# Optimization experiments

Hardware: AMD Instinct MI355X
Metric: run time of the kernel (lower is better)

Reference implementation:

```python
import jax, jax.numpy as jnp
import numpy as np

D_MODEL, H, D_FF = 512, 8, 2048
DK = D_MODEL // H
EPS = 1e-5  # torch LayerNorm default


def layer_norm(x, g, b):
    m = jnp.mean(x, axis=-1, keepdims=True)
    v = jnp.mean((x - m) ** 2, axis=-1, keepdims=True)
    return (x - m) * jax.lax.rsqrt(v + EPS) * g + b


def setup_inputs() -> dict:
    key = jax.random.key(0)
    ks = jax.random.split(key, 10)
    B, S = 8, 2048
    s = lambda fan_in: 1.0 / np.sqrt(fan_in)
    return {
        "x": jax.random.normal(ks[0], (B, S, D_MODEL), jnp.float32),
        # per-head projections stacked: [h, d_model, dk] (bias-free Project)
        "wq": jax.random.uniform(ks[1], (H, D_MODEL, DK), jnp.float32, -s(D_MODEL), s(D_MODEL)),
        "wk": jax.random.uniform(ks[2], (H, D_MODEL, DK), jnp.float32, -s(D_MODEL), s(D_MODEL)),
        "wv": jax.random.uniform(ks[3], (H, D_MODEL, DK), jnp.float32, -s(D_MODEL), s(D_MODEL)),
        "wo": jax.random.uniform(ks[4], (D_MODEL, D_MODEL), jnp.float32, -s(D_MODEL), s(D_MODEL)),
        "w1": jax.random.uniform(ks[5], (D_MODEL, D_FF), jnp.float32, -s(D_MODEL), s(D_MODEL)),
        "b1": jax.random.uniform(ks[6], (D_FF,), jnp.float32, -s(D_MODEL), s(D_MODEL)),
        "w2": jax.random.uniform(ks[7], (D_FF, D_MODEL), jnp.float32, -s(D_FF), s(D_FF)),
        "b2": jax.random.uniform(ks[8], (D_MODEL,), jnp.float32, -s(D_FF), s(D_FF)),
        "ln1_g": jnp.ones((D_MODEL,), jnp.float32),
        "ln1_b": jnp.zeros((D_MODEL,), jnp.float32),
        "ln2_g": jnp.ones((D_MODEL,), jnp.float32),
        "ln2_b": jnp.zeros((D_MODEL,), jnp.float32),
    }


def reference(x, wq, wk, wv, wo, w1, b1, w2, b2, ln1_g, ln1_b, ln2_g, ln2_b):
    B, S, D = x.shape
    # --- multi-head self-attention (8 per-head Linears fused into one einsum) ---
    q = jnp.einsum("bsd,hdk->bhsk", x, wq)
    k = jnp.einsum("bsd,hdk->bhsk", x, wk)
    v = jnp.einsum("bsd,hdk->bhsk", x, wv)
    score = jnp.einsum("bhsk,bhtk->bhst", q, k) * (1.0 / np.sqrt(DK))
    attn = jax.nn.softmax(score, axis=-1)
    heads = jnp.einsum("bhst,bhtk->bhsk", attn, v)
    concat = heads.transpose(0, 2, 1, 3).reshape(B, S, D)  # cat over heads
    mha = concat @ wo
    # dropout in eval mode -> identity
    x = layer_norm(mha + x, ln1_g, ln1_b)
    # --- feed-forward ---
    ffn = jax.nn.relu(x @ w1 + b1) @ w2 + b2
    return layer_norm(ffn + x, ln2_g, ln2_b)
```

## Files before the change

### kernel.cpp

```cpp
#include <hip/hip_runtime.h>
#include <hip/hip_bf16.h>
#include <math.h>


#define D_MODEL 512
#define NHEAD   8
#define DKH     64
#define SEQ     2048
#define BATCH   8
#define DFF     2048
#define MROWS   (BATCH * SEQ)
#define QKVLD   1536

typedef __bf16 bf16x8 __attribute__((ext_vector_type(8)));
typedef float  f32x4  __attribute__((ext_vector_type(4)));

__device__ __forceinline__ unsigned short f2bf(float f) {
    union { float f; unsigned u; } v; v.f = f;
    return (unsigned short)((v.u + 0x7FFFu + ((v.u >> 16) & 1u)) >> 16);
}

__device__ __forceinline__ unsigned cvtpk(float a, float b) {
    unsigned r;
    asm("v_cvt_pk_bf16_f32 %0, %1, %2" : "=v"(r) : "v"(a), "v"(b));
    return r;
}

__device__ __forceinline__ float fexp2(float x) {
    float r; asm("v_exp_f32 %0, %1" : "=v"(r) : "v"(x)); return r;
}

__device__ __forceinline__ f32x4 mfma16(bf16x8 a, bf16x8 b, f32x4 c) {
    return __builtin_amdgcn_mfma_f32_16x16x32_bf16(a, b, c, 0, 0, 0);
}

__device__ __forceinline__ void gld_lds16(const unsigned short* g, unsigned short* l) {
    __builtin_amdgcn_global_load_lds(
        (const __attribute__((address_space(1))) unsigned int*)g,
        (__attribute__((address_space(3))) unsigned int*)l, 16, 0, 0);
}

template<bool BIAS, bool RELU, bool RES, bool OUTF32>
__global__ __launch_bounds__(256)
void mfma_gemm(const unsigned short* __restrict__ Av,
               const unsigned short* __restrict__ Bt,
               const float* __restrict__ bias, const float* __restrict__ res,
               void* __restrict__ Cv, int Kdim, int lda, int ldc)
{
    __shared__ unsigned short As[2][128][32];
    __shared__ unsigned short Bs[2][128][32];

    const int tid  = threadIdx.x;
    const int lane = tid & 63;
    const int w    = tid >> 6;
    const int mq   = (w >> 1) << 6;
    const int nq   = (w & 1) << 6;
    const int lrow = lane & 15;
    const int g    = lane >> 4;
    const int lk   = g << 3;

    const int row0 = blockIdx.y << 7;
    const int col0 = blockIdx.x << 7;

    const int c0   = w << 5;
    const int srow = lane >> 2;
    const int scol = (lane & 3) << 3;
    const size_t aoff = (size_t)(row0 + c0 + srow) * lda  + scol;
    const size_t boff = (size_t)(col0 + c0 + srow) * Kdim + scol;

    auto stage = [&](int buf, int kt) {
        gld_lds16(Av + aoff + kt,                        &As[buf][c0     ][0]);
        gld_lds16(Av + aoff + (size_t)16 * lda  + kt,    &As[buf][c0 + 16][0]);
        gld_lds16(Bt + boff + kt,                        &Bs[buf][c0     ][0]);
        gld_lds16(Bt + boff + (size_t)16 * Kdim + kt,    &Bs[buf][c0 + 16][0]);
    };

    const f32x4 zero = {0.f, 0.f, 0.f, 0.f};
    f32x4 acc[4][4];
    #pragma unroll
    for (int i = 0; i < 4; ++i)
        #pragma unroll
        for (int j = 0; j < 4; ++j) acc[i][j] = zero;

    stage(0, 0);
    __syncthreads();

    int cur = 0;
    for (int kt = 0; kt < Kdim; kt += 32) {
        if (kt + 32 < Kdim) stage(cur ^ 1, kt + 32);

        bf16x8 af[4], bfv[4];
        #pragma unroll
        for (int mf = 0; mf < 4; ++mf)
            af[mf] = *(const bf16x8*)&As[cur][mq + mf * 16 + lrow][lk];
        #pragma unroll
        for (int nf = 0; nf < 4; ++nf)
            bfv[nf] = *(const bf16x8*)&Bs[cur][nq + nf * 16 + lrow][lk];
        #pragma unroll
        for (int mf = 0; mf < 4; ++mf)
            #pragma unroll
            for (int nf = 0; nf < 4; ++nf)
                acc[mf][nf] = mfma16(af[mf], bfv[nf], acc[mf][nf]);

        __syncthreads();
        cur ^= 1;
    }

    const int orow = row0 + mq + g * 4;
    const int ocol = col0 + nq + lrow;
    #pragma unroll
    for (int mf = 0; mf < 4; ++mf) {
        #pragma unroll
        for (int nf = 0; nf < 4; ++nf) {
            const int cc = ocol + nf * 16;
            float bv = 0.f;
            if constexpr (BIAS) bv = bias[cc];
            float v[4];
            #pragma unroll
            for (int r = 0; r < 4; ++r) {
                const int rr = orow + mf * 16 + r;
                v[r] = acc[mf][nf][r];
                if constexpr (BIAS) v[r] += bv;
                if constexpr (RELU) v[r] = fmaxf(v[r], 0.f);
                if constexpr (RES)  v[r] += res[(size_t)rr * ldc + cc];
                if constexpr (OUTF32) ((float*)Cv)[(size_t)rr * ldc + cc] = v[r];
            }
            if constexpr (!OUTF32) {
                const unsigned u01 = cvtpk(v[0], v[1]);
                const unsigned u23 = cvtpk(v[2], v[3]);
                unsigned short* cp = (unsigned short*)Cv + (size_t)(orow + mf * 16) * ldc + cc;
                cp[0]                 = (unsigned short)u01;
                cp[(size_t)ldc]       = (unsigned short)(u01 >> 16);
                cp[(size_t)ldc * 2]   = (unsigned short)u23;
                cp[(size_t)ldc * 3]   = (unsigned short)(u23 >> 16);
            }
        }
    }
}

__global__ __launch_bounds__(512)
void mfma_attn(unsigned short* __restrict__ qkv)
{
    __shared__ unsigned short Ks[64][72];
    __shared__ unsigned short Vt[64][72];
    __shared__ unsigned short Ps[128][76];

    const int tid  = threadIdx.x;
    const int lane = tid & 63;
    const int w    = tid >> 6;
    const int lrow = lane & 15;
    const int g    = lane >> 4;
    const int lk   = g << 3;

    const int bid  = blockIdx.x;
    const int slot = bid >> 3;
    const int bh   = (bid & 7) * 8 + (slot & 7);
    const int b  = bh >> 3, h = bh & 7;
    const int s0 = (slot >> 3) << 7;

    unsigned short* qptr = qkv + ((size_t)(b * SEQ + s0)) * QKVLD + h * DKH;
    const unsigned short* kbase = qkv + ((size_t)(b * SEQ)) * QKVLD + 512 + h * DKH;
    const unsigned short* vbase = qkv + ((size_t)(b * SEQ)) * QKVLD + 1024 + h * DKH;

    bf16x8 qf[2];
    {
        const unsigned short* qp = qptr + (size_t)(w * 16 + lrow) * QKVLD;
        qf[0] = *(const bf16x8*)(qp + lk);
        qf[1] = *(const bf16x8*)(qp + 32 + lk);
    }

    const int kr = tid >> 3, kc = (tid & 7) << 3;
    const int vr = lane,     vc = w << 3;

    uint4 kreg, vreg;
    auto loadKV = [&](int t0) {
        kreg = *(const uint4*)(kbase + (size_t)(t0 + kr) * QKVLD + kc);
        vreg = *(const uint4*)(vbase + (size_t)(t0 + vr) * QKVLD + vc);
    };
    loadKV(0);

    const f32x4 zero = {0.f, 0.f, 0.f, 0.f};
    f32x4 oacc[4];
    float mrun[4], lpart[4];
    #pragma unroll
    for (int i = 0; i < 4; ++i) { oacc[i] = zero; mrun[i] = -INFINITY; lpart[i] = 0.f; }

    for (int t0 = 0; t0 < SEQ; t0 += 64) {
        __syncthreads();
        *(uint4*)&Ks[kr][kc] = kreg;
        {
            const unsigned short* vu = (const unsigned short*)&vreg;
            #pragma unroll
            for (int j = 0; j < 8; ++j) Vt[vc + j][vr] = vu[j];
        }
        __syncthreads();

        if (t0 + 64 < SEQ) loadKV(t0 + 64);

        f32x4 sacc[4];
        #pragma unroll
        for (int nf = 0; nf < 4; ++nf) sacc[nf] = zero;
        __builtin_amdgcn_s_setprio(1);
        #pragma unroll
        for (int kk = 0; kk < 2; ++kk) {
            #pragma unroll
            for (int nf = 0; nf < 4; ++nf) {
                const bf16x8 kf = *(const bf16x8*)&Ks[nf * 16 + lrow][kk * 32 + lk];
                sacc[nf] = mfma16(qf[kk], kf, sacc[nf]);
            }
        }
        __builtin_amdgcn_s_setprio(0);

        float pmax[4];
        bool need = false;
        #pragma unroll
        for (int r = 0; r < 4; ++r) {
            pmax[r] = fmaxf(fmaxf(sacc[0][r], sacc[1][r]),
                            fmaxf(sacc[2][r], sacc[3][r]));
            need |= (pmax[r] > mrun[r] + 8.f);
        }
        if (__any(need)) {
            #pragma unroll
            for (int r = 0; r < 4; ++r) {
                float mt = pmax[r];
                mt = fmaxf(mt, __shfl_xor(mt, 1, 16));
                mt = fmaxf(mt, __shfl_xor(mt, 2, 16));
                mt = fmaxf(mt, __shfl_xor(mt, 4, 16));
                mt = fmaxf(mt, __shfl_xor(mt, 8, 16));
                const float mnew = fmaxf(mrun[r], mt);
                const float alpha = fexp2(mrun[r] - mnew);
                mrun[r] = mnew;
                lpart[r] *= alpha;
                #pragma unroll
                for (int nf = 0; nf < 4; ++nf) oacc[nf][r] *= alpha;
            }
        }
        #pragma unroll
        for (int r = 0; r < 4; ++r) {
            const float p0 = fexp2(sacc[0][r] - mrun[r]);
            const float p1 = fexp2(sacc[1][r] - mrun[r]);
            const float p2 = fexp2(sacc[2][r] - mrun[r]);
            const float p3 = fexp2(sacc[3][r] - mrun[r]);
            lpart[r] += (p0 + p1) + (p2 + p3);
            const unsigned u01 = cvtpk(p0, p1);
            const unsigned u23 = cvtpk(p2, p3);
            unsigned short* prow = &Ps[w * 16 + g * 4 + r][lrow];
            prow[0]  = (unsigned short)u01;
            prow[16] = (unsigned short)(u01 >> 16);
            prow[32] = (unsigned short)u23;
            prow[48] = (unsigned short)(u23 >> 16);
        }

        __builtin_amdgcn_s_setprio(1);
        #pragma unroll
        for (int kk = 0; kk < 2; ++kk) {
            const bf16x8 pf = *(const bf16x8*)&Ps[w * 16 + lrow][kk * 32 + lk];
            #pragma unroll
            for (int nf = 0; nf < 4; ++nf) {
                const bf16x8 vf = *(const bf16x8*)&Vt[nf * 16 + lrow][kk * 32 + lk];
                oacc[nf] = mfma16(pf, vf, oacc[nf]);
            }
        }
        __builtin_amdgcn_s_setprio(0);
    }

    #pragma unroll
    for (int r = 0; r < 4; ++r) {
        float l = lpart[r];
        l += __shfl_xor(l, 1, 16);
        l += __shfl_xor(l, 2, 16);
        l += __shfl_xor(l, 4, 16);
        l += __shfl_xor(l, 8, 16);
        const float inv = 1.f / l;
        #pragma unroll
        for (int nf = 0; nf < 4; ++nf)
            qptr[(size_t)(w * 16 + g * 4 + r) * QKVLD + nf * 16 + lrow] =
                f2bf(oacc[nf][r] * inv);
    }
}

template<bool WB>
__global__ __launch_bounds__(256)
void ln_kernel(const float* __restrict__ in, const float* __restrict__ gg,
               const float* __restrict__ bb, float* __restrict__ outf,
               unsigned short* __restrict__ outb)
{
    const int row = blockIdx.x * 4 + (threadIdx.x >> 6);
    const int lane = threadIdx.x & 63;
    const float* p = in + (size_t)row * D_MODEL;

    const float4 a = *(const float4*)(p + lane * 4);
    const float4 c = *(const float4*)(p + 256 + lane * 4);
    float sum = a.x + a.y + a.z + a.w + c.x + c.y + c.z + c.w;
    float sq  = a.x*a.x + a.y*a.y + a.z*a.z + a.w*a.w
              + c.x*c.x + c.y*c.y + c.z*c.z + c.w*c.w;
    #pragma unroll
    for (int msk = 1; msk < 64; msk <<= 1) {
        sum += __shfl_xor(sum, msk, 64);
        sq  += __shfl_xor(sq,  msk, 64);
    }
    const float mean = sum * (1.f / 512.f);
    const float var  = sq * (1.f / 512.f) - mean * mean;
    const float rs   = rsqrtf(var + 1e-5f);

    const float4 g0 = *(const float4*)(gg + lane * 4);
    const float4 g1 = *(const float4*)(gg + 256 + lane * 4);
    const float4 b0 = *(const float4*)(bb + lane * 4);
    const float4 b1 = *(const float4*)(bb + 256 + lane * 4);

    float4 o0, o1;
    o0.x = (a.x - mean) * rs * g0.x + b0.x;
    o0.y = (a.y - mean) * rs * g0.y + b0.y;
    o0.z = (a.z - mean) * rs * g0.z + b0.z;
    o0.w = (a.w - mean) * rs * g0.w + b0.w;
    o1.x = (c.x - mean) * rs * g1.x + b1.x;
    o1.y = (c.y - mean) * rs * g1.y + b1.y;
    o1.z = (c.z - mean) * rs * g1.z + b1.z;
    o1.w = (c.w - mean) * rs * g1.w + b1.w;
    *(float4*)(outf + (size_t)row * D_MODEL + lane * 4) = o0;
    *(float4*)(outf + (size_t)row * D_MODEL + 256 + lane * 4) = o1;
    if constexpr (WB) {
        uint2 pa, pb;
        pa.x = cvtpk(o0.x, o0.y);
        pa.y = cvtpk(o0.z, o0.w);
        pb.x = cvtpk(o1.x, o1.y);
        pb.y = cvtpk(o1.z, o1.w);
        *(uint2*)(outb + (size_t)row * D_MODEL + lane * 4) = pa;
        *(uint2*)(outb + (size_t)row * D_MODEL + 256 + lane * 4) = pb;
    }
}

__global__ __launch_bounds__(256)
void cast_bf16(const float* __restrict__ in, unsigned short* __restrict__ out)
{
    const size_t i = ((size_t)blockIdx.x * 256 + threadIdx.x) * 8;
    const float4 a = *(const float4*)(in + i);
    const float4 b = *(const float4*)(in + i + 4);
    uint4 o;
    o.x = cvtpk(a.x, a.y);
    o.y = cvtpk(a.z, a.w);
    o.z = cvtpk(b.x, b.y);
    o.w = cvtpk(b.z, b.w);
    *(uint4*)(out + i) = o;
}

__global__ __launch_bounds__(256)
void pack_qkv(const float* __restrict__ wq, const float* __restrict__ wk,
              const float* __restrict__ wv, unsigned short* __restrict__ Wqkv)
{
    const int idx = blockIdx.x * 256 + threadIdx.x;
    const int n = idx >> 9, d = idx & 511;
    const int h = n >> 6, c = n & 63;
    const size_t src = ((size_t)h * 512 + d) * 64 + c;
    Wqkv[idx]                 = f2bf(wq[src] * 0.18033688f);
    Wqkv[idx + 512 * 512]     = f2bf(wk[src]);
    Wqkv[idx + 2 * 512 * 512] = f2bf(wv[src]);
}

__global__ __launch_bounds__(256)
void pack_t(const float* __restrict__ in, unsigned short* __restrict__ out,
            int K, int N)
{
    const int idx = blockIdx.x * 256 + threadIdx.x;
    const int n = idx / K, k = idx % K;
    out[idx] = f2bf(in[(size_t)k * N + n]);
}

extern "C" void kernel_launch(void* const* d_in, const int* in_sizes, int n_in,
                              void* d_out, int out_size, void* d_ws, size_t ws_size,
                              hipStream_t stream)
{
    (void)in_sizes; (void)n_in; (void)out_size;

    const float* x    = (const float*)d_in[0];
    const float* wq   = (const float*)d_in[1];
    const float* wk   = (const float*)d_in[2];
    const float* wv   = (const float*)d_in[3];
    const float* wo   = (const float*)d_in[4];
    const float* w1   = (const float*)d_in[5];
    const float* b1   = (const float*)d_in[6];
    const float* w2   = (const float*)d_in[7];
    const float* b2   = (const float*)d_in[8];
    const float* ln1g = (const float*)d_in[9];
    const float* ln1b = (const float*)d_in[10];
    const float* ln2g = (const float*)d_in[11];
    const float* ln2b = (const float*)d_in[12];
    float* out = (float*)d_out;

    const size_t QKV_BYTES = (size_t)MROWS * QKVLD * 2;
    const size_t Y_BYTES   = (size_t)MROWS * D_MODEL * 4;
    unsigned char* base = (unsigned char*)d_ws;
    unsigned short* qkv  = (unsigned short*)(base);
    float*          y    = (float*)(base + QKV_BYTES);
    unsigned short* Wqkv = (unsigned short*)(base + QKV_BYTES + Y_BYTES);
    unsigned short* wo_t = Wqkv + 3 * 512 * 512;
    unsigned short* w1_t = wo_t + 512 * 512;
    unsigned short* w2_t = w1_t + 2048 * 512;
    unsigned short* hid  = w2_t + 2048 * 512;

    const size_t hid_off = (size_t)((unsigned char*)hid - base);
    const size_t avail = (ws_size > hid_off) ? (ws_size - hid_off) : 0;
    int chunk = (int)(avail / ((size_t)DFF * 2));
    chunk &= ~127;
    if (chunk > MROWS) chunk = MROWS;
    if (chunk < 128)   chunk = 128;

    float* y2 = (float*)qkv;
    unsigned short* xb  = (unsigned short*)d_out;
    unsigned short* x1b = (unsigned short*)d_out;

    pack_qkv<<<1024, 256, 0, stream>>>(wq, wk, wv, Wqkv);
    pack_t<<<(512 * 512) / 256, 256, 0, stream>>>(wo, wo_t, 512, 512);
    pack_t<<<(2048 * 512) / 256, 256, 0, stream>>>(w1, w1_t, 512, 2048);
    pack_t<<<(2048 * 512) / 256, 256, 0, stream>>>(w2, w2_t, 2048, 512);
    cast_bf16<<<(MROWS * D_MODEL) / (256 * 8), 256, 0, stream>>>(x, xb);

    const dim3 blk(256);

    mfma_gemm<false, false, false, false>
        <<<dim3(12, MROWS / 128), blk, 0, stream>>>(xb, Wqkv, nullptr, nullptr,
                                                    qkv, 512, 512, QKVLD);

    mfma_attn<<<dim3(1024), dim3(512), 0, stream>>>(qkv);

    mfma_gemm<false, false, true, true>
        <<<dim3(4, MROWS / 128), blk, 0, stream>>>(qkv, wo_t, nullptr, x, y,
                                                   512, QKVLD, 512);

    ln_kernel<true><<<MROWS / 4, blk, 0, stream>>>(y, ln1g, ln1b, y, x1b);

    for (int r0 = 0; r0 < MROWS; r0 += chunk) {
        const int rows = (r0 + chunk <= MROWS) ? chunk : (MROWS - r0);
        mfma_gemm<true, true, false, false>
            <<<dim3(DFF / 128, rows / 128), blk, 0, stream>>>(
                x1b + (size_t)r0 * D_MODEL, w1_t, b1, nullptr, hid,
                512, 512, DFF);
        mfma_gemm<true, false, true, true>
            <<<dim3(4, rows / 128), blk, 0, stream>>>(
                hid, w2_t, b2, y + (size_t)r0 * D_MODEL,
                y2 + (size_t)r0 * D_MODEL, DFF, DFF, 512);
    }

    ln_kernel<false><<<MROWS / 4, blk, 0, stream>>>(y2, ln2g, ln2b, out, nullptr);
}
```

Baseline: 350.3 us.

## Process 256 query rows per attention block with two Q sub-tiles per warp

Each warp in the attention kernel now handles two 16-row query sub-tiles, so a block covers 256 queries and the grid halves to 512 blocks. Every K/V tile staged in shared memory is therefore reused for twice as many MFMAs, cutting K/V global loads and LDS staging per unit of work. The P store is changed to a permuted 8-byte vector write, with a matching column permutation of the V transpose, and launch bounds now request higher occupancy. In exchange, register pressure roughly doubles for accumulators, and with fewer blocks there is a risk of occupancy loss or poor CU utilisation.

After: 311.7 us. 11.0% less time.

```diff
diff --git a/kernel.cpp b/kernel.cpp
--- a/kernel.cpp
+++ b/kernel.cpp
@@ -138,12 +138,54 @@
     }
 }
 
-__global__ __launch_bounds__(512)
+__device__ __forceinline__ void softmax_store(
+    f32x4* sacc, float* mrun, float* lpart, f32x4* oacc,
+    unsigned short (*Ps)[76], int rowbase, int g, int lrow)
+{
+    float pmax[4];
+    bool need = false;
+    #pragma unroll
+    for (int r = 0; r < 4; ++r) {
+        pmax[r] = fmaxf(fmaxf(sacc[0][r], sacc[1][r]),
+                        fmaxf(sacc[2][r], sacc[3][r]));
+        need |= (pmax[r] > mrun[r] + 8.f);
+    }
+    if (__any(need)) {
+        #pragma unroll
+        for (int r = 0; r < 4; ++r) {
+            float mt = pmax[r];
+            mt = fmaxf(mt, __shfl_xor(mt, 1, 16));
+            mt = fmaxf(mt, __shfl_xor(mt, 2, 16));
+            mt = fmaxf(mt, __shfl_xor(mt, 4, 16));
+            mt = fmaxf(mt, __shfl_xor(mt, 8, 16));
+            const float mnew = fmaxf(mrun[r], mt);
+            const float alpha = fexp2(mrun[r] - mnew);
+            mrun[r] = mnew;
+            lpart[r] *= alpha;
+            #pragma unroll
+            for (int nf = 0; nf < 4; ++nf) oacc[nf][r] *= alpha;
+        }
+    }
+    #pragma unroll
+    for (int r = 0; r < 4; ++r) {
+        const float p0 = fexp2(sacc[0][r] - mrun[r]);
+        const float p1 = fexp2(sacc[1][r] - mrun[r]);
+        const float p2 = fexp2(sacc[2][r] - mrun[r]);
+        const float p3 = fexp2(sacc[3][r] - mrun[r]);
+        lpart[r] += (p0 + p1) + (p2 + p3);
+        uint2 u;
+        u.x = cvtpk(p0, p1);
+        u.y = cvtpk(p2, p3);
+        *(uint2*)&Ps[rowbase + g * 4 + r][4 * lrow] = u;
+    }
+}
+
+__global__ __launch_bounds__(512, 4)
 void mfma_attn(unsigned short* __restrict__ qkv)
 {
     __shared__ unsigned short Ks[64][72];
     __shared__ unsigned short Vt[64][72];
-    __shared__ unsigned short Ps[128][76];
+    __shared__ unsigned short Ps[256][76];
 
     const int tid  = threadIdx.x;
     const int lane = tid & 63;
@@ -153,24 +195,26 @@
     const int lk   = g << 3;
 
     const int bid  = blockIdx.x;
-    const int slot = bid >> 3;
-    const int bh   = (bid & 7) * 8 + (slot & 7);
+    const int idx  = bid >> 3;
+    const int bh   = (bid & 7) * 8 + (idx & 7);
     const int b  = bh >> 3, h = bh & 7;
-    const int s0 = (slot >> 3) << 7;
+    const int s0 = (idx >> 3) << 8;
 
     unsigned short* qptr = qkv + ((size_t)(b * SEQ + s0)) * QKVLD + h * DKH;
     const unsigned short* kbase = qkv + ((size_t)(b * SEQ)) * QKVLD + 512 + h * DKH;
     const unsigned short* vbase = qkv + ((size_t)(b * SEQ)) * QKVLD + 1024 + h * DKH;
 
-    bf16x8 qf[2];
-    {
-        const unsigned short* qp = qptr + (size_t)(w * 16 + lrow) * QKVLD;
-        qf[0] = *(const bf16x8*)(qp + lk);
-        qf[1] = *(const bf16x8*)(qp + 32 + lk);
+    bf16x8 qf[2][2];
+    #pragma unroll
+    for (int sub = 0; sub < 2; ++sub) {
+        const unsigned short* qp = qptr + (size_t)(w * 32 + sub * 16 + lrow) * QKVLD;
+        qf[sub][0] = *(const bf16x8*)(qp + lk);
+        qf[sub][1] = *(const bf16x8*)(qp + 32 + lk);
     }
 
     const int kr = tid >> 3, kc = (tid & 7) << 3;
-    const int vr = lane,     vc = w << 3;
+    const int vr = tid & 63, vc = (tid >> 6) << 3;
+    const int cvr = ((vr & 15) << 2) | (vr >> 4);
 
     uint4 kreg, vreg;
     auto loadKV = [&](int t0) {
@@ -180,10 +224,13 @@
     loadKV(0);
 
     const f32x4 zero = {0.f, 0.f, 0.f, 0.f};
-    f32x4 oacc[4];
-    float mrun[4], lpart[4];
-    #pragma unroll
-    for (int i = 0; i < 4; ++i) { oacc[i] = zero; mrun[i] = -INFINITY; lpart[i] = 0.f; }
+    f32x4 oacc0[4], oacc1[4];
+    float m0[4], l0[4], m1[4], l1[4];
+    #pragma unroll
+    for (int i = 0; i < 4; ++i) {
+        oacc0[i] = zero; oacc1[i] = zero;
+        m0[i] = -INFINITY; m1[i] = -INFINITY; l0[i] = 0.f; l1[i] = 0.f;
+    }
 
     for (int t0 = 0; t0 < SEQ; t0 += 64) {
         __syncthreads();
@@ -191,74 +238,40 @@
         {
             const unsigned short* vu = (const unsigned short*)&vreg;
             #pragma unroll
-            for (int j = 0; j < 8; ++j) Vt[vc + j][vr] = vu[j];
+            for (int j = 0; j < 8; ++j) Vt[vc + j][cvr] = vu[j];
         }
         __syncthreads();
 
         if (t0 + 64 < SEQ) loadKV(t0 + 64);
 
-        f32x4 sacc[4];
-        #pragma unroll
-        for (int nf = 0; nf < 4; ++nf) sacc[nf] = zero;
+        f32x4 s0a[4], s1a[4];
+        #pragma unroll
+        for (int nf = 0; nf < 4; ++nf) { s0a[nf] = zero; s1a[nf] = zero; }
         __builtin_amdgcn_s_setprio(1);
         #pragma unroll
         for (int kk = 0; kk < 2; ++kk) {
             #pragma unroll
             for (int nf = 0; nf < 4; ++nf) {
                 const bf16x8 kf = *(const bf16x8*)&Ks[nf * 16 + lrow][kk * 32 + lk];
-                sacc[nf] = mfma16(qf[kk], kf, sacc[nf]);
+                s0a[nf] = mfma16(qf[0][kk], kf, s0a[nf]);
+                s1a[nf] = mfma16(qf[1][kk], kf, s1a[nf]);
             }
         }
         __builtin_amdgcn_s_setprio(0);
 
-        float pmax[4];
-        bool need = false;
-        #pragma unroll
-        for (int r = 0; r < 4; ++r) {
-            pmax[r] = fmaxf(fmaxf(sacc[0][r], sacc[1][r]),
-                            fmaxf(sacc[2][r], sacc[3][r]));
-            need |= (pmax[r] > mrun[r] + 8.f);
-        }
-        if (__any(need)) {
-            #pragma unroll
-            for (int r = 0; r < 4; ++r) {
-                float mt = pmax[r];
-                mt = fmaxf(mt, __shfl_xor(mt, 1, 16));
-                mt = fmaxf(mt, __shfl_xor(mt, 2, 16));
-                mt = fmaxf(mt, __shfl_xor(mt, 4, 16));
-                mt = fmaxf(mt, __shfl_xor(mt, 8, 16));
-                const float mnew = fmaxf(mrun[r], mt);
-                const float alpha = fexp2(mrun[r] - mnew);
-                mrun[r] = mnew;
-                lpart[r] *= alpha;
-                #pragma unroll
-                for (int nf = 0; nf < 4; ++nf) oacc[nf][r] *= alpha;
-            }
-        }
-        #pragma unroll
-        for (int r = 0; r < 4; ++r) {
-            const float p0 = fexp2(sacc[0][r] - mrun[r]);
-            const float p1 = fexp2(sacc[1][r] - mrun[r]);
-            const float p2 = fexp2(sacc[2][r] - mrun[r]);
-            const float p3 = fexp2(sacc[3][r] - mrun[r]);
-            lpart[r] += (p0 + p1) + (p2 + p3);
-            const unsigned u01 = cvtpk(p0, p1);
-            const unsigned u23 = cvtpk(p2, p3);
-            unsigned short* prow = &Ps[w * 16 + g * 4 + r][lrow];
-            prow[0]  = (unsigned short)u01;
-            prow[16] = (unsigned short)(u01 >> 16);
-            prow[32] = (unsigned short)u23;
-            prow[48] = (unsigned short)(u23 >> 16);
-        }
+        softmax_store(s0a, m0, l0, oacc0, Ps, w * 32,      g, lrow);
+        softmax_store(s1a, m1, l1, oacc1, Ps, w * 32 + 16, g, lrow);
 
         __builtin_amdgcn_s_setprio(1);
         #pragma unroll
         for (int kk = 0; kk < 2; ++kk) {
-            const bf16x8 pf = *(const bf16x8*)&Ps[w * 16 + lrow][kk * 32 + lk];
+            const bf16x8 pf0 = *(const bf16x8*)&Ps[w * 32 + lrow][kk * 32 + lk];
+            const bf16x8 pf1 = *(const bf16x8*)&Ps[w * 32 + 16 + lrow][kk * 32 + lk];
             #pragma unroll
             for (int nf = 0; nf < 4; ++nf) {
                 const bf16x8 vf = *(const bf16x8*)&Vt[nf * 16 + lrow][kk * 32 + lk];
-                oacc[nf] = mfma16(pf, vf, oacc[nf]);
+                oacc0[nf] = mfma16(pf0, vf, oacc0[nf]);
+                oacc1[nf] = mfma16(pf1, vf, oacc1[nf]);
             }
         }
         __builtin_amdgcn_s_setprio(0);
@@ -266,7 +279,7 @@
 
     #pragma unroll
     for (int r = 0; r < 4; ++r) {
-        float l = lpart[r];
+        float l = l0[r];
         l += __shfl_xor(l, 1, 16);
         l += __shfl_xor(l, 2, 16);
         l += __shfl_xor(l, 4, 16);
@@ -274,8 +287,21 @@
         const float inv = 1.f / l;
         #pragma unroll
         for (int nf = 0; nf < 4; ++nf)
-            qptr[(size_t)(w * 16 + g * 4 + r) * QKVLD + nf * 16 + lrow] =
-                f2bf(oacc[nf][r] * inv);
+            qptr[(size_t)(w * 32 + g * 4 + r) * QKVLD + nf * 16 + lrow] =
+                f2bf(oacc0[nf][r] * inv);
+    }
+    #pragma unroll
+    for (int r = 0; r < 4; ++r) {
+        float l = l1[r];
+        l += __shfl_xor(l, 1, 16);
+        l += __shfl_xor(l, 2, 16);
+        l += __shfl_xor(l, 4, 16);
+        l += __shfl_xor(l, 8, 16);
+        const float inv = 1.f / l;
+        #pragma unroll
+        for (int nf = 0; nf < 4; ++nf)
+            qptr[(size_t)(w * 32 + 16 + g * 4 + r) * QKVLD + nf * 16 + lrow] =
+                f2bf(oacc1[nf][r] * inv);
     }
 }
 
@@ -421,7 +447,7 @@
         <<<dim3(12, MROWS / 128), blk, 0, stream>>>(xb, Wqkv, nullptr, nullptr,
                                                     qkv, 512, 512, QKVLD);
 
-    mfma_attn<<<dim3(1024), dim3(512), 0, stream>>>(qkv);
+    mfma_attn<<<dim3(512), dim3(512), 0, stream>>>(qkv);
 
     mfma_gemm<false, false, true, true>
         <<<dim3(4, MROWS / 128), blk, 0, stream>>>(qkv, wo_t, nullptr, x, y,
```
